# Kernel optimization log

Measured on AMD Instinct MI355X. Metric: run time of the kernel, lower is better.

The kernel has to match this reference:

```python
import jax, jax.numpy as jnp
import numpy as np

NUM_NODES = 64
NUM_FEATURES = 256
OUTPUT_DIM = 256
BATCH_GRAPHS = 4096
TOTAL_ROWS = NUM_NODES * BATCH_GRAPHS


def setup_inputs() -> dict:
    key = jax.random.key(0)
    kx, kw = jax.random.split(key)
    x = jax.random.normal(kx, (TOTAL_ROWS, NUM_FEATURES), dtype=jnp.float32)
    # row i belongs to graph i // NUM_NODES (matches stride-num_nodes indexing in the module)
    batch = jnp.arange(TOTAL_ROWS, dtype=jnp.int64) // NUM_NODES
    # per-node linear weights: mlp[inode] is o3.Linear(256x0e -> 256x0e), bias-free
    W = jax.random.normal(kw, (NUM_NODES, NUM_FEATURES, OUTPUT_DIM), dtype=jnp.float32)
    return {"x": x, "batch": batch, "W": W}


def reference(x, batch, W):
    # x: [B*num_nodes, F]; W: [num_nodes, F, O]
    num_nodes, F, _ = W.shape
    B = x.shape[0] // num_nodes
    # node_features_reshape: out[b, :, inode] = x[inode + b*num_nodes] == reshape(B, num_nodes, F)
    xr = x.reshape(B, num_nodes, F)
    scale = 1.0 / jnp.sqrt(jnp.asarray(F, dtype=x.dtype))  # o3.Linear path normalization
    out = jnp.einsum("bnf,nfo->bno", xr, W) * scale  # per-node batched GEMM
    # scatter back: outs[inode + b*num_nodes] = out[b, inode] == reshape
    return out.reshape(B * num_nodes, -1)
```

## Files before the change

kernel.cpp:

```cpp
#include <hip/hip_runtime.h>
#include <stdint.h>

#define NODES   64
#define FDIM    256
#define ODIM    256
#define BGRAPH  4096
#define TROWS   (NODES * BGRAPH)

#define BM 128
#define BN 256
#define BK 32
#define ASTRIDE 40

typedef short  bf16x8  __attribute__((ext_vector_type(8)));
typedef float  floatx4 __attribute__((ext_vector_type(4)));

__device__ inline unsigned short f2bf(float f) {
    unsigned int u = __float_as_uint(f);
    return (unsigned short)((u + 0x7fffu + ((u >> 16) & 1u)) >> 16);
}

__global__ __launch_bounds__(256) void transpose_w(const float* __restrict__ W,
                                                   unsigned short* __restrict__ Wt) {
    __shared__ unsigned short t[64][65];
    const int node = blockIdx.y;
    const int tf = (blockIdx.x >> 2) << 6;
    const int to = (blockIdx.x & 3) << 6;
    const int tid = threadIdx.x;
    const float* Wn = W + node * (FDIM * ODIM);
#pragma unroll
    for (int i = 0; i < 16; ++i) {
        int flat = i * 256 + tid;
        int r = flat >> 6, c = flat & 63;
        float v = Wn[(tf + r) * ODIM + (to + c)] * 0.0625f;
        t[c][r] = f2bf(v);
    }
    __syncthreads();
    unsigned short* Wtn = Wt + node * (FDIM * ODIM);
#pragma unroll
    for (int i = 0; i < 16; ++i) {
        int flat = i * 256 + tid;
        int r = flat >> 6, c = flat & 63;
        Wtn[(to + r) * FDIM + (tf + c)] = t[r][c];
    }
}

__global__ __launch_bounds__(256, 2) void gemm_node(const float* __restrict__ x,
                                                    const unsigned short* __restrict__ Wt,
                                                    float* __restrict__ out) {
    __shared__ unsigned short As[2][BM * ASTRIDE];
    __shared__ unsigned short Bs[2][BN * BK];

    const int bid  = blockIdx.x;
    const int xcd  = bid & 7;
    const int jj   = bid >> 3;
    const int node = xcd * 8 + (jj & 7);
    const int mblk = jj >> 3;
    const int b0   = mblk * BM;

    const int tid  = threadIdx.x;
    const int lane = tid & 63;
    const int wave = tid >> 6;
    const int wm   = wave >> 1;
    const int wn   = wave & 1;
    const int l15  = lane & 15;
    const int l4   = lane >> 4;

    const float* xblk = x + ((size_t)b0 * NODES + node) * FDIM;
    const unsigned short* wt_node = Wt + (size_t)node * (ODIM * FDIM);

    int arow[4], ach[4];
    size_t aoff[4];
#pragma unroll
    for (int i = 0; i < 4; ++i) {
        int q = i * 256 + tid;
        arow[i] = q >> 3;
        ach[i]  = q & 7;
        aoff[i] = (size_t)arow[i] * (NODES * FDIM) + ach[i] * 4;
    }

    floatx4 acc[4][8] = {};
    float4 av[4];

#pragma unroll
    for (int i = 0; i < 4; ++i) av[i] = *(const float4*)(xblk + aoff[i]);
#pragma unroll
    for (int j = 0; j < 4; ++j) {
        const int slot_base = (wave * 4 + j) * 64;
        const int s = slot_base + lane;
        const int o = s >> 2, c = s & 3;
        const int jg = c ^ ((o >> 1) & 3);
        const unsigned short* g = wt_node + (size_t)o * FDIM + jg * 8;
        __builtin_amdgcn_global_load_lds(
            (const __attribute__((address_space(1))) void*)g,
            (__attribute__((address_space(3))) void*)(&Bs[0][slot_base * 8]),
            16, 0, 0);
    }
#pragma unroll
    for (int i = 0; i < 4; ++i) {
        ushort4 p;
        p.x = f2bf(av[i].x); p.y = f2bf(av[i].y); p.z = f2bf(av[i].z); p.w = f2bf(av[i].w);
        *(ushort4*)(&As[0][arow[i] * ASTRIDE + ach[i] * 4]) = p;
    }
    __syncthreads();

#pragma unroll
    for (int kt = 0; kt < 8; ++kt) {
        const int cur = kt & 1, nxt = cur ^ 1;
        const int k1 = (kt + 1) * BK;

        if (kt < 7) {
#pragma unroll
            for (int i = 0; i < 4; ++i) av[i] = *(const float4*)(xblk + aoff[i] + k1);
#pragma unroll
            for (int j = 0; j < 4; ++j) {
                const int slot_base = (wave * 4 + j) * 64;
                const int s = slot_base + lane;
                const int o = s >> 2, c = s & 3;
                const int jg = c ^ ((o >> 1) & 3);
                const unsigned short* g = wt_node + (size_t)o * FDIM + k1 + jg * 8;
                __builtin_amdgcn_global_load_lds(
                    (const __attribute__((address_space(1))) void*)g,
                    (__attribute__((address_space(3))) void*)(&Bs[nxt][slot_base * 8]),
                    16, 0, 0);
            }
        }

        bf16x8 a[4], b[8];
#pragma unroll
        for (int mi = 0; mi < 4; ++mi) {
            const int m = wm * 64 + mi * 16 + l15;
            a[mi] = *(const bf16x8*)(&As[cur][m * ASTRIDE + l4 * 8]);
        }
#pragma unroll
        for (int ni = 0; ni < 8; ++ni) {
            const int n = wn * 128 + ni * 16 + l15;
            b[ni] = *(const bf16x8*)(&Bs[cur][n * 32 + (l4 ^ ((n >> 1) & 3)) * 8]);
        }

#pragma unroll
        for (int mi = 0; mi < 4; ++mi)
#pragma unroll
            for (int ni = 0; ni < 8; ++ni)
                acc[mi][ni] = __builtin_amdgcn_mfma_f32_16x16x32_bf16(a[mi], b[ni], acc[mi][ni], 0, 0, 0);

        if (kt < 7) {
#pragma unroll
            for (int i = 0; i < 4; ++i) {
                ushort4 p;
                p.x = f2bf(av[i].x); p.y = f2bf(av[i].y); p.z = f2bf(av[i].z); p.w = f2bf(av[i].w);
                *(ushort4*)(&As[nxt][arow[i] * ASTRIDE + ach[i] * 4]) = p;
            }
            __syncthreads();
        }
    }

    float* outblk = out + ((size_t)b0 * NODES + node) * ODIM;
#pragma unroll
    for (int mi = 0; mi < 4; ++mi) {
        const int row_base = wm * 64 + mi * 16 + l4 * 4;
#pragma unroll
        for (int ni = 0; ni < 8; ++ni) {
            const int col = wn * 128 + ni * 16 + l15;
#pragma unroll
            for (int r = 0; r < 4; ++r) {
                outblk[(size_t)(row_base + r) * (NODES * ODIM) + col] = acc[mi][ni][r];
            }
        }
    }
}

__global__ __launch_bounds__(256) void naive_kernel(const float* __restrict__ x,
                                                    const float* __restrict__ W,
                                                    float* __restrict__ out) {
    __shared__ float xs[FDIM];
    const int row = blockIdx.x;
    const int node = row & (NODES - 1);
    const int o = threadIdx.x;
    xs[o] = x[(size_t)row * FDIM + o];
    __syncthreads();
    const float* Wn = W + (size_t)node * FDIM * ODIM;
    float s = 0.f;
#pragma unroll 8
    for (int f = 0; f < FDIM; ++f) s += xs[f] * Wn[(size_t)f * ODIM + o];
    out[(size_t)row * ODIM + o] = s * 0.0625f;
}

extern "C" void kernel_launch(void* const* d_in, const int* in_sizes, int n_in,
                              void* d_out, int out_size, void* d_ws, size_t ws_size,
                              hipStream_t stream) {
    const float* x = (const float*)d_in[0];
    const float* W = (const float*)d_in[2];
    float* out = (float*)d_out;

    const size_t wt_bytes = (size_t)NODES * ODIM * FDIM * sizeof(unsigned short);
    if (ws_size >= wt_bytes) {
        unsigned short* Wt = (unsigned short*)d_ws;
        transpose_w<<<dim3(16, NODES), 256, 0, stream>>>(W, Wt);
        gemm_node<<<dim3((BGRAPH / BM) * NODES), 256, 0, stream>>>(x, Wt, out);
    } else {
        naive_kernel<<<dim3(TROWS), 256, 0, stream>>>(x, W, out);
    }
}
```

Measured before the change: 464.3 us.

## Load full-K bf16 A tile into swizzled LDS upfront with BM halved

Halves the M tile to 64 rows and loads each block's entire 64x256 slice of x at once, converts it to bf16 and stores it into an XOR-swizzled LDS buffer, so the K loop only streams the weight tiles. This removes the per-iteration global x loads and the conversion from the main loop and doubles the block count. In exchange, every x load is issued before the first MFMA with no overlap, and each block re-streams the full per-node weight matrix for half as many rows, which doubles total weight traffic.

```diff
diff --git a/kernel.cpp b/kernel.cpp
--- a/kernel.cpp
+++ b/kernel.cpp
@@ -7,10 +7,9 @@
 #define BGRAPH  4096
 #define TROWS   (NODES * BGRAPH)
 
-#define BM 128
+#define BM 64
 #define BN 256
 #define BK 32
-#define ASTRIDE 40
 
 typedef short  bf16x8  __attribute__((ext_vector_type(8)));
 typedef float  floatx4 __attribute__((ext_vector_type(4)));
@@ -48,8 +47,8 @@
 __global__ __launch_bounds__(256, 2) void gemm_node(const float* __restrict__ x,
                                                     const unsigned short* __restrict__ Wt,
                                                     float* __restrict__ out) {
-    __shared__ unsigned short As[2][BM * ASTRIDE];
-    __shared__ unsigned short Bs[2][BN * BK];
+    __shared__ __align__(16) unsigned short As[BM * 256];
+    __shared__ __align__(16) unsigned short Bs[2][BN * BK];
 
     const int bid  = blockIdx.x;
     const int xcd  = bid & 7;
@@ -69,21 +68,6 @@
     const float* xblk = x + ((size_t)b0 * NODES + node) * FDIM;
     const unsigned short* wt_node = Wt + (size_t)node * (ODIM * FDIM);
 
-    int arow[4], ach[4];
-    size_t aoff[4];
-#pragma unroll
-    for (int i = 0; i < 4; ++i) {
-        int q = i * 256 + tid;
-        arow[i] = q >> 3;
-        ach[i]  = q & 7;
-        aoff[i] = (size_t)arow[i] * (NODES * FDIM) + ach[i] * 4;
-    }
-
-    floatx4 acc[4][8] = {};
-    float4 av[4];
-
-#pragma unroll
-    for (int i = 0; i < 4; ++i) av[i] = *(const float4*)(xblk + aoff[i]);
 #pragma unroll
     for (int j = 0; j < 4; ++j) {
         const int slot_base = (wave * 4 + j) * 64;
@@ -96,22 +80,27 @@
             (__attribute__((address_space(3))) void*)(&Bs[0][slot_base * 8]),
             16, 0, 0);
     }
+
 #pragma unroll
-    for (int i = 0; i < 4; ++i) {
+    for (int i = 0; i < 16; ++i) {
+        const int q = i * 256 + tid;
+        const int r = q >> 6, ch = q & 63;
+        const float4 v = *(const float4*)(xblk + (size_t)r * (NODES * FDIM) + ch * 4);
         ushort4 p;
-        p.x = f2bf(av[i].x); p.y = f2bf(av[i].y); p.z = f2bf(av[i].z); p.w = f2bf(av[i].w);
-        *(ushort4*)(&As[0][arow[i] * ASTRIDE + ach[i] * 4]) = p;
+        p.x = f2bf(v.x); p.y = f2bf(v.y); p.z = f2bf(v.z); p.w = f2bf(v.w);
+        const int slot = (ch >> 1) ^ (r & 7);
+        *(ushort4*)(&As[r * 256 + slot * 8 + (ch & 1) * 4]) = p;
     }
     __syncthreads();
+
+    floatx4 acc[2][8] = {};
 
 #pragma unroll
     for (int kt = 0; kt < 8; ++kt) {
         const int cur = kt & 1, nxt = cur ^ 1;
-        const int k1 = (kt + 1) * BK;
 
         if (kt < 7) {
-#pragma unroll
-            for (int i = 0; i < 4; ++i) av[i] = *(const float4*)(xblk + aoff[i] + k1);
+            const int k1 = (kt + 1) * BK;
 #pragma unroll
             for (int j = 0; j < 4; ++j) {
                 const int slot_base = (wave * 4 + j) * 64;
@@ -126,11 +115,12 @@
             }
         }
 
-        bf16x8 a[4], b[8];
+        bf16x8 a[2], b[8];
 #pragma unroll
-        for (int mi = 0; mi < 4; ++mi) {
-            const int m = wm * 64 + mi * 16 + l15;
-            a[mi] = *(const bf16x8*)(&As[cur][m * ASTRIDE + l4 * 8]);
+        for (int mi = 0; mi < 2; ++mi) {
+            const int m = wm * 32 + mi * 16 + l15;
+            const int slot = (kt * 4 + l4) ^ (m & 7);
+            a[mi] = *(const bf16x8*)(&As[m * 256 + slot * 8]);
         }
 #pragma unroll
         for (int ni = 0; ni < 8; ++ni) {
@@ -139,26 +129,18 @@
         }
 
 #pragma unroll
-        for (int mi = 0; mi < 4; ++mi)
+        for (int mi = 0; mi < 2; ++mi)
 #pragma unroll
             for (int ni = 0; ni < 8; ++ni)
                 acc[mi][ni] = __builtin_amdgcn_mfma_f32_16x16x32_bf16(a[mi], b[ni], acc[mi][ni], 0, 0, 0);
 
-        if (kt < 7) {
-#pragma unroll
-            for (int i = 0; i < 4; ++i) {
-                ushort4 p;
-                p.x = f2bf(av[i].x); p.y = f2bf(av[i].y); p.z = f2bf(av[i].z); p.w = f2bf(av[i].w);
-                *(ushort4*)(&As[nxt][arow[i] * ASTRIDE + ach[i] * 4]) = p;
-            }
-            __syncthreads();
-        }
+        if (kt < 7) __syncthreads();
     }
 
     float* outblk = out + ((size_t)b0 * NODES + node) * ODIM;
 #pragma unroll
-    for (int mi = 0; mi < 4; ++mi) {
-        const int row_base = wm * 64 + mi * 16 + l4 * 4;
+    for (int mi = 0; mi < 2; ++mi) {
+        const int row_base = wm * 32 + mi * 16 + l4 * 4;
 #pragma unroll
         for (int ni = 0; ni < 8; ++ni) {
             const int col = wn * 128 + ni * 16 + l15;
```

After: 462.2 us. About the same (-0.5%).
